# Kernel optimization log

Measured on AMD Instinct MI355X. Metric: run time of the kernel, lower is better.

## Reference

```python
import jax, jax.numpy as jnp
import numpy as np

B, S, H = 2, 2048, 2048
NQ, NKV = 32, 8          # query heads, kv heads
G = NQ // NKV            # query groups per kv head
D = H // NQ              # head dim = 64
MAX_POS = 4096
THETA = 10000.0


def _rope_tables(position_ids):
    # freqs per the original apply_rotary_emb (interleaved pair convention)
    freqs = 1.0 / THETA ** (jnp.arange(0, D, 2)[: D // 2].astype(jnp.float32) / D)
    t = jnp.arange(MAX_POS, dtype=jnp.float32)
    ang = jnp.outer(t, freqs)                     # [MAX_POS, D/2]
    cos = jnp.take(jnp.cos(ang), position_ids, axis=0)[:, :, None, :]  # [B,S,1,D/2]
    sin = jnp.take(jnp.sin(ang), position_ids, axis=0)[:, :, None, :]
    return cos, sin


def _apply_rope(x, cos, sin):
    # x: [B,S,h,D]; pairs are interleaved (x0,x1),(x2,x3),...
    x2 = x.astype(jnp.float32).reshape(*x.shape[:-1], D // 2, 2)
    xr, xi = x2[..., 0], x2[..., 1]
    out_r = xr * cos - xi * sin
    out_i = xr * sin + xi * cos
    return jnp.stack((out_r, out_i), axis=-1).reshape(x.shape).astype(x.dtype)


def setup_inputs() -> dict:
    key = jax.random.key(0)
    ks = jax.random.split(key, 5)
    init_scale = 0.02 / np.sqrt(H)
    hidden_states = jax.random.normal(ks[0], (B, S, H), dtype=jnp.float32)
    wq = jax.random.normal(ks[1], (H, H), dtype=jnp.float32) * init_scale
    wk = jax.random.normal(ks[2], (H, H // G), dtype=jnp.float32) * init_scale
    wv = jax.random.normal(ks[3], (H, H // G), dtype=jnp.float32) * init_scale
    wo = jax.random.normal(ks[4], (H, H), dtype=jnp.float32) * init_scale
    attention_mask = jnp.ones((B, S), dtype=jnp.int32)
    position_ids = jnp.broadcast_to(jnp.arange(S, dtype=jnp.int32), (B, S))
    return dict(hidden_states=hidden_states, attention_mask=attention_mask,
                position_ids=position_ids, wq=wq, wk=wk, wv=wv, wo=wo)


def reference(hidden_states, attention_mask, position_ids, wq, wk, wv, wo):
    # projections (no bias)
    xq = (hidden_states @ wq).reshape(B, S, NQ, D)
    xk = (hidden_states @ wk).reshape(B, S, NKV, D)
    xv = (hidden_states @ wv).reshape(B, S, NKV, D)
    # GQA repeat: kv head h -> query heads h*G .. h*G+G-1 (consecutive)
    xk = jnp.repeat(xk, G, axis=2)  # [B,S,NQ,D]
    xv = jnp.repeat(xv, G, axis=2)

    cos, sin = _rope_tables(position_ids)
    xq = _apply_rope(xq, cos, sin)
    xk = _apply_rope(xk, cos, sin)

    # causal + padding mask -> additive bias
    causal = jnp.tril(jnp.ones((S, S), dtype=bool))[None, None]          # [1,1,S,S]
    pad = (attention_mask > 0)[:, None, None, :]                          # [B,1,1,S]
    combined = jnp.logical_and(causal, pad)                               # [B,1,S,S]
    neg = jnp.finfo(jnp.float32).min
    bias = jnp.where(combined, 0.0, neg).astype(jnp.float32)

    scale = 1.0 / np.sqrt(D)
    scores = jnp.einsum('bqhd,bkhd->bhqk', xq, xk).astype(jnp.float32) * scale
    scores = scores + bias
    attn = jax.nn.softmax(scores, axis=-1)                                # [B,NQ,S,S] fp32
    out = jnp.einsum('bhqk,bkhd->bqhd', attn, xv)                         # [B,S,NQ,D]
    out = out.reshape(B, S, H)
    return out @ wo
```

## Files before the change

kernel.cpp:

```cpp
#include <hip/hip_runtime.h>
#include <cstdint>

typedef __attribute__((ext_vector_type(8))) __bf16  bf8v;
typedef __attribute__((ext_vector_type(4))) float   f4v;
typedef __attribute__((ext_vector_type(8))) unsigned short ush8;

__device__ __forceinline__ float bf2f(unsigned short u) {
    union { unsigned u; float f; } v; v.u = ((unsigned)u) << 16; return v.f;
}
__device__ __forceinline__ unsigned short f2bf(float f) {
    union { float f; unsigned u; } v; v.f = f;
    unsigned u = v.u;
    return (unsigned short)((u + 0x7fffu + ((u >> 16) & 1u)) >> 16);
}
__device__ __forceinline__ unsigned short f2bf_n(float f) {
    union { __bf16 h; unsigned short s; } v; v.h = (__bf16)f; return v.s;
}
__device__ __forceinline__ unsigned pack2bf(float a, float b) {
    union { __bf16 h[2]; unsigned u; } v;
    v.h[0] = (__bf16)a; v.h[1] = (__bf16)b; return v.u;
}

#define GLDS16(gp, lp)                                                          \
    __builtin_amdgcn_global_load_lds(                                           \
        (const __attribute__((address_space(1))) void*)(uintptr_t)(gp),         \
        (__attribute__((address_space(3))) void*)(uintptr_t)(lp), 16, 0, 0)

__global__ void cast_f32_to_bf16(const float* __restrict__ in,
                                 unsigned short* __restrict__ out, int n8) {
    int i = blockIdx.x * 256 + threadIdx.x;
    if (i >= n8) return;
    float4 a = ((const float4*)in)[2 * i];
    float4 b = ((const float4*)in)[2 * i + 1];
    ush8 o;
    o[0] = f2bf(a.x); o[1] = f2bf(a.y); o[2] = f2bf(a.z); o[3] = f2bf(a.w);
    o[4] = f2bf(b.x); o[5] = f2bf(b.y); o[6] = f2bf(b.z); o[7] = f2bf(b.w);
    ((ush8*)out)[i] = o;
}

__global__ void transpose_cast(const float* __restrict__ in,
                               unsigned short* __restrict__ out, int R, int C) {
    __shared__ float t[32][33];
    int c0 = blockIdx.x * 32, r0 = blockIdx.y * 32;
    int x = threadIdx.x, y = threadIdx.y;
    #pragma unroll
    for (int i = 0; i < 32; i += 8) t[y + i][x] = in[(size_t)(r0 + y + i) * C + c0 + x];
    __syncthreads();
    #pragma unroll
    for (int i = 0; i < 32; i += 8)
        out[(size_t)(c0 + y + i) * R + r0 + x] = f2bf(t[x][y + i]);
}

__global__ void transpose_v_bf16(const unsigned short* __restrict__ in,
                                 unsigned short* __restrict__ out) {
    __shared__ unsigned short t[32][33];
    int c0 = blockIdx.x * 32;
    int r0 = blockIdx.y * 32;
    int x = threadIdx.x, y = threadIdx.y;
    #pragma unroll
    for (int i = 0; i < 32; i += 8)
        t[y + i][x] = in[(size_t)(r0 + y + i) * 3072 + 2560 + c0 + x];
    __syncthreads();
    #pragma unroll
    for (int i = 0; i < 32; i += 8)
        out[(size_t)(c0 + y + i) * 4096 + r0 + x] = t[x][y + i];
}

__global__ void rope_strided(unsigned short* __restrict__ X,
                             const int* __restrict__ pos_ids,
                             int coloff, int stride, int nh_log2) {
    int idx = blockIdx.x * 256 + threadIdx.x;
    int i   = idx & 31;
    int hh  = (idx >> 5) & ((1 << nh_log2) - 1);
    int tok = idx >> (5 + nh_log2);
    int pos = pos_ids[tok];
    float ang = (float)pos * exp2f(-0.41524101186092f * (float)i);
    float s = sinf(ang), c = cosf(ang);
    unsigned short* p = X + (size_t)tok * stride + coloff + hh * 64 + 2 * i;
    unsigned pr = *(const unsigned*)p;
    float xr = bf2f((unsigned short)(pr & 0xffff));
    float xi = bf2f((unsigned short)(pr >> 16));
    float orr = xr * c - xi * s;
    float oi  = xr * s + xi * c;
    *(unsigned*)p = (unsigned)f2bf(orr) | ((unsigned)f2bf(oi) << 16);
}

template <int OUT_BF16>
__global__ __launch_bounds__(256) void gemm_bt(const unsigned short* __restrict__ A,
                                               const unsigned short* __restrict__ Bt,
                                               void* __restrict__ Cv, int N, int K) {
    __shared__ __align__(16) unsigned short As[128 * 64];
    __shared__ __align__(16) unsigned short Bs[128 * 64];
    const int t = threadIdx.x;
    const int lane = t & 63, w = t >> 6;
    const int wr = w >> 1, wc = w & 1;
    const int lr = lane & 15, lh = lane >> 4;
    const int m0 = blockIdx.y * 128, n0 = blockIdx.x * 128;

    f4v acc[4][4];
    #pragma unroll
    for (int i = 0; i < 4; ++i)
        #pragma unroll
        for (int j = 0; j < 4; ++j) acc[i][j] = f4v{0.f, 0.f, 0.f, 0.f};

    const int o_t = t * 16;
    for (int k0 = 0; k0 < K; k0 += 64) {
        __syncthreads();
        #pragma unroll
        for (int s = 0; s < 4; ++s) {
            int o = s * 4096 + o_t;
            int row = o >> 7;
            int src = (o & 127) ^ ((row & 7) << 4);
            const unsigned short* gA = A + (size_t)(m0 + row) * K + k0 + (src >> 1);
            GLDS16(gA, As + (o >> 1));
            const unsigned short* gB = Bt + (size_t)(n0 + row) * K + k0 + (src >> 1);
            GLDS16(gB, Bs + (o >> 1));
        }
        __syncthreads();
        #pragma unroll
        for (int kk = 0; kk < 2; ++kk) {
            bf8v af[4], bfr[4];
            #pragma unroll
            for (int mi = 0; mi < 4; ++mi) {
                int row = wr * 64 + mi * 16 + lr;
                int col = (kk * 32 + lh * 8) ^ ((row & 7) << 3);
                af[mi] = *(const bf8v*)(As + row * 64 + col);
            }
            #pragma unroll
            for (int ni = 0; ni < 4; ++ni) {
                int row = wc * 64 + ni * 16 + lr;
                int col = (kk * 32 + lh * 8) ^ ((row & 7) << 3);
                bfr[ni] = *(const bf8v*)(Bs + row * 64 + col);
            }
            #pragma unroll
            for (int mi = 0; mi < 4; ++mi)
                #pragma unroll
                for (int ni = 0; ni < 4; ++ni)
                    acc[mi][ni] = __builtin_amdgcn_mfma_f32_16x16x32_bf16(
                        af[mi], bfr[ni], acc[mi][ni], 0, 0, 0);
        }
    }
    #pragma unroll
    for (int mi = 0; mi < 4; ++mi)
        #pragma unroll
        for (int ni = 0; ni < 4; ++ni)
            #pragma unroll
            for (int r = 0; r < 4; ++r) {
                int row = m0 + wr * 64 + mi * 16 + lh * 4 + r;
                int col = n0 + wc * 64 + ni * 16 + lr;
                float v = acc[mi][ni][r];
                if (OUT_BF16) ((unsigned short*)Cv)[(size_t)row * N + col] = f2bf(v);
                else          ((float*)Cv)[(size_t)row * N + col] = v;
            }
}

__global__ __launch_bounds__(256, 4) void flash_attn(
        const unsigned short* __restrict__ QKV,
        const unsigned short* __restrict__ VtG,
        const int* __restrict__ amask,
        const int* __restrict__ pos_ids,
        unsigned short* __restrict__ O) {
    __shared__ __align__(16) unsigned short Ks[2][64 * 64];
    __shared__ __align__(16) unsigned short Vs[2][64 * 64];
    __shared__ __align__(16) unsigned short Ps[4][16 * 64];
    __shared__ int aliveT[32];

    const int t = threadIdx.x, lane = t & 63, w = t >> 6;
    const int lr = lane & 15, lh = lane >> 4;
    const int pair = blockIdx.x, h = blockIdx.y, b = blockIdx.z;
    const size_t tok0 = (size_t)b * 2048;

    const unsigned short* Kb = QKV + tok0 * 3072 + 2048 + (h >> 2) * 64;
    const unsigned short* Vb = VtG + (size_t)((h >> 2) * 64) * 4096 + tok0;
    const int* amrow = amask + b * 2048;

#define STAGE(buf, kt)                                                              \
    {   _Pragma("unroll")                                                           \
        for (int s_ = 0; s_ < 2; ++s_) {                                            \
            int c_ = s_ * 256 + t;                                                  \
            int row_ = c_ >> 3;                                                     \
            int sc_ = (((c_ & 7) * 16) ^ ((row_ & 7) << 4)) >> 1;                   \
            GLDS16(Kb + (size_t)((kt) * 64 + row_) * 3072 + sc_, Ks[buf] + c_ * 8); \
            GLDS16(Vb + (size_t)row_ * 4096 + (kt) * 64 + sc_, Vs[buf] + c_ * 8);   \
        }                                                                           \
    }

    const float SCL = 0.18033688011112042f;
    int cur = 0;

    if (t < 32) aliveT[t] = -1;
    __syncthreads();
    {
        const int4* am4 = (const int4*)amrow;
        int4 a0 = am4[2 * t], a1 = am4[2 * t + 1];
        int f = (a0.x && a0.y && a0.z && a0.w && a1.x && a1.y && a1.z && a1.w) ? -1 : 0;
        atomicAnd(&aliveT[t >> 3], f);
    }

    #pragma unroll 1
    for (int half = 0; half < 2; ++half) {
        const int qt = half ? (31 - pair) : pair;
        const int q0 = qt * 64;
        const int nkv = qt + 1;
        const int qloc = w * 16 + lr;

        const unsigned short* Qp = QKV + (tok0 + q0 + qloc) * 3072 + h * 64;
        union Q8 { bf8v v; unsigned short s[8]; } qa0u, qa1u;
        qa0u.v = *(const bf8v*)(Qp + lh * 8);
        qa1u.v = *(const bf8v*)(Qp + 32 + lh * 8);
        {
            int pos = pos_ids[tok0 + q0 + qloc];
            #pragma unroll
            for (int r = 0; r < 4; ++r) {
                float i0 = (float)(lh * 4 + r);
                float ang0 = (float)pos * exp2f(-0.41524101186092f * i0);
                float sn = sinf(ang0), cs = cosf(ang0);
                float xr = bf2f(qa0u.s[2 * r]), xi = bf2f(qa0u.s[2 * r + 1]);
                qa0u.s[2 * r]     = f2bf_n((xr * cs - xi * sn) * SCL);
                qa0u.s[2 * r + 1] = f2bf_n((xr * sn + xi * cs) * SCL);
                float i1 = (float)(16 + lh * 4 + r);
                float ang1 = (float)pos * exp2f(-0.41524101186092f * i1);
                float sn1 = sinf(ang1), cs1 = cosf(ang1);
                float yr = bf2f(qa1u.s[2 * r]), yi = bf2f(qa1u.s[2 * r + 1]);
                qa1u.s[2 * r]     = f2bf_n((yr * cs1 - yi * sn1) * SCL);
                qa1u.s[2 * r + 1] = f2bf_n((yr * sn1 + yi * cs1) * SCL);
            }
        }
        const bf8v qa0 = qa0u.v, qa1 = qa1u.v;

        f4v oacc[4];
        #pragma unroll
        for (int i = 0; i < 4; ++i) oacc[i] = f4v{0.f, 0.f, 0.f, 0.f};
        float m_ = -1e30f, l_ = 0.f;

        STAGE(cur, 0);
        __syncthreads();

        #pragma unroll 1
        for (int kt = 0; kt < nkv; ++kt) {
            if (kt + 1 < nkv) STAGE(cur ^ 1, kt + 1);

            f4v sa[4];
            #pragma unroll
            for (int kf = 0; kf < 4; ++kf) sa[kf] = f4v{0.f, 0.f, 0.f, 0.f};
            __builtin_amdgcn_s_setprio(1);
            #pragma unroll
            for (int kk = 0; kk < 2; ++kk) {
                bf8v qa = kk ? qa1 : qa0;
                int col = kk * 32 + lh * 8;
                #pragma unroll
                for (int kf = 0; kf < 4; ++kf) {
                    bf8v kb = *(const bf8v*)(Ks[cur] + (kf * 16 + lr) * 64 + (col ^ ((lr & 7) << 3)));
                    sa[kf] = __builtin_amdgcn_mfma_f32_16x16x32_bf16(kb, qa, sa[kf], 0, 0, 0);
                }
            }
            __builtin_amdgcn_s_setprio(0);

            const bool diag = (kt == qt);
            const bool tileAlive = (aliveT[kt] != 0);

            float pvv[4][4];
            if (tileAlive && !diag) {
                #pragma unroll
                for (int kf = 0; kf < 4; ++kf)
                    #pragma unroll
                    for (int r = 0; r < 4; ++r) pvv[kf][r] = sa[kf][r];
            } else if (tileAlive) {
                #pragma unroll
                for (int kf = 0; kf < 4; ++kf)
                    #pragma unroll
                    for (int r = 0; r < 4; ++r) {
                        int keyl = kf * 16 + lh * 4 + r;
                        pvv[kf][r] = (keyl > qloc) ? -1e30f : sa[kf][r];
                    }
            } else {
                int amv[4][4];
                #pragma unroll
                for (int kf = 0; kf < 4; ++kf) {
                    int4 aq = *(const int4*)(amrow + kt * 64 + kf * 16 + lh * 4);
                    amv[kf][0] = aq.x; amv[kf][1] = aq.y; amv[kf][2] = aq.z; amv[kf][3] = aq.w;
                }
                #pragma unroll
                for (int kf = 0; kf < 4; ++kf)
                    #pragma unroll
                    for (int r = 0; r < 4; ++r) {
                        int keyl = kf * 16 + lh * 4 + r;
                        bool dead = (amv[kf][r] == 0) || (diag && keyl > qloc);
                        pvv[kf][r] = dead ? -1e30f : sa[kf][r];
                    }
            }

            float t0 = fmaxf(fmaxf(pvv[0][0], pvv[0][1]), fmaxf(pvv[0][2], pvv[0][3]));
            float t1 = fmaxf(fmaxf(pvv[1][0], pvv[1][1]), fmaxf(pvv[1][2], pvv[1][3]));
            float t2 = fmaxf(fmaxf(pvv[2][0], pvv[2][1]), fmaxf(pvv[2][2], pvv[2][3]));
            float t3 = fmaxf(fmaxf(pvv[3][0], pvv[3][1]), fmaxf(pvv[3][2], pvv[3][3]));
            float mx = fmaxf(fmaxf(t0, t1), fmaxf(t2, t3));
            mx = fmaxf(mx, __shfl_xor(mx, 16));
            mx = fmaxf(mx, __shfl_xor(mx, 32));

            if (!__all(mx <= m_ + 8.0f)) {
                float mn = fmaxf(m_, mx);
                float fac = exp2f(m_ - mn);
                m_ = mn;
                l_ *= fac;
                float facr[4];
                #pragma unroll
                for (int r = 0; r < 4; ++r) facr[r] = __shfl(fac, lh * 4 + r);
                #pragma unroll
                for (int df = 0; df < 4; ++df) {
                    f4v o = oacc[df];
                    o[0] *= facr[0]; o[1] *= facr[1]; o[2] *= facr[2]; o[3] *= facr[3];
                    oacc[df] = o;
                }
            }

            float pe[4][4];
            #pragma unroll
            for (int kf = 0; kf < 4; ++kf)
                #pragma unroll
                for (int r = 0; r < 4; ++r)
                    pe[kf][r] = exp2f(pvv[kf][r] - m_);
            float s0 = (pe[0][0] + pe[0][1]) + (pe[0][2] + pe[0][3]);
            float s1 = (pe[1][0] + pe[1][1]) + (pe[1][2] + pe[1][3]);
            float s2 = (pe[2][0] + pe[2][1]) + (pe[2][2] + pe[2][3]);
            float s3 = (pe[3][0] + pe[3][1]) + (pe[3][2] + pe[3][3]);
            float rs = (s0 + s1) + (s2 + s3);
            rs += __shfl_xor(rs, 16);
            rs += __shfl_xor(rs, 32);
            l_ += rs;

            unsigned short* Pw = Ps[w];
            #pragma unroll
            for (int kf = 0; kf < 4; ++kf) {
                uint2 pk;
                pk.x = pack2bf(pe[kf][0], pe[kf][1]);
                pk.y = pack2bf(pe[kf][2], pe[kf][3]);
                int idx = lr * 64 + ((kf * 16 + lh * 4) ^ ((lr & 7) << 3));
                *(uint2*)(Pw + idx) = pk;
            }

            __builtin_amdgcn_s_setprio(1);
            #pragma unroll
            for (int kk = 0; kk < 2; ++kk) {
                int k0c = kk * 32 + lh * 8;
                bf8v pa = *(const bf8v*)(Pw + lr * 64 + (k0c ^ ((lr & 7) << 3)));
                #pragma unroll
                for (int df = 0; df < 4; ++df) {
                    int d = df * 16 + lr;
                    bf8v vb = *(const bf8v*)(Vs[cur] + d * 64 + (k0c ^ ((d & 7) << 3)));
                    oacc[df] = __builtin_amdgcn_mfma_f32_16x16x32_bf16(pa, vb, oacc[df], 0, 0, 0);
                }
            }
            __builtin_amdgcn_s_setprio(0);

            __syncthreads();
            cur ^= 1;
        }

        float invl = 1.0f / l_;
        float invr[4];
        #pragma unroll
        for (int r = 0; r < 4; ++r) invr[r] = __shfl(invl, lh * 4 + r);
        #pragma unroll
        for (int df = 0; df < 4; ++df)
            #pragma unroll
            for (int r = 0; r < 4; ++r) {
                int qg = q0 + w * 16 + lh * 4 + r;
                float v = oacc[df][r] * invr[r];
                O[(tok0 + qg) * 2048 + h * 64 + df * 16 + lr] = f2bf_n(v);
            }
    }
#undef STAGE
}

extern "C" void kernel_launch(void* const* d_in, const int* in_sizes, int n_in,
                              void* d_out, int out_size, void* d_ws, size_t ws_size,
                              hipStream_t stream) {
    const float* hs   = (const float*)d_in[0];
    const int* amask  = (const int*)d_in[1];
    const int* pos    = (const int*)d_in[2];
    const float* wq   = (const float*)d_in[3];
    const float* wk   = (const float*)d_in[4];
    const float* wv   = (const float*)d_in[5];
    const float* wo   = (const float*)d_in[6];

    char* ws = (char*)d_ws;
    unsigned short* Xb   = (unsigned short*)(ws);
    unsigned short* Wqkv = (unsigned short*)(ws + 16777216);
    unsigned short* Wot  = (unsigned short*)(ws + 29360128);
    unsigned short* AOb  = (unsigned short*)(ws + 37748736);

    char* ob = (char*)d_out;
    unsigned short* QKV = (unsigned short*)ob;
    unsigned short* VtG = (unsigned short*)(ob + 25165824);

    cast_f32_to_bf16<<<4096, 256, 0, stream>>>(hs, Xb, 1048576);
    transpose_cast<<<dim3(64, 64), dim3(32, 8), 0, stream>>>(wq, Wqkv, 2048, 2048);
    transpose_cast<<<dim3(16, 64), dim3(32, 8), 0, stream>>>(wk, Wqkv + 4194304, 2048, 512);
    transpose_cast<<<dim3(16, 64), dim3(32, 8), 0, stream>>>(wv, Wqkv + 5242880, 2048, 512);
    transpose_cast<<<dim3(64, 64), dim3(32, 8), 0, stream>>>(wo, Wot, 2048, 2048);

    gemm_bt<1><<<dim3(24, 32), 256, 0, stream>>>(Xb, Wqkv, (void*)QKV, 3072, 2048);

    rope_strided<<<4096, 256, 0, stream>>>(QKV, pos, 2048, 3072, 3);

    transpose_v_bf16<<<dim3(16, 128), dim3(32, 8), 0, stream>>>(QKV, VtG);

    flash_attn<<<dim3(16, 32, 2), 256, 0, stream>>>(QKV, VtG, amask, pos, AOb);

    gemm_bt<0><<<dim3(16, 32), 256, 0, stream>>>(AOb, Wot, d_out, 2048, 2048);
}
```

Measured before the change: 241.6 us.

## Feed P directly from registers via 16x16x16 MFMA, drop P LDS staging

```diff
diff --git a/kernel.cpp b/kernel.cpp
--- a/kernel.cpp
+++ b/kernel.cpp
@@ -3,6 +3,7 @@
 
 typedef __attribute__((ext_vector_type(8))) __bf16  bf8v;
 typedef __attribute__((ext_vector_type(4))) float   f4v;
+typedef __attribute__((ext_vector_type(4))) short   s4v;
 typedef __attribute__((ext_vector_type(8))) unsigned short ush8;
 
 __device__ __forceinline__ float bf2f(unsigned short u) {
@@ -154,7 +155,7 @@
             }
 }
 
-__global__ __launch_bounds__(256, 4) void flash_attn(
+__global__ __launch_bounds__(256, 5) void flash_attn(
         const unsigned short* __restrict__ QKV,
         const unsigned short* __restrict__ VtG,
         const int* __restrict__ amask,
@@ -162,8 +163,6 @@
         unsigned short* __restrict__ O) {
     __shared__ __align__(16) unsigned short Ks[2][64 * 64];
     __shared__ __align__(16) unsigned short Vs[2][64 * 64];
-    __shared__ __align__(16) unsigned short Ps[4][16 * 64];
-    __shared__ int aliveT[32];
 
     const int t = threadIdx.x, lane = t & 63, w = t >> 6;
     const int lr = lane & 15, lh = lane >> 4;
@@ -186,16 +185,27 @@
     }
 
     const float SCL = 0.18033688011112042f;
-    int cur = 0;
-
-    if (t < 32) aliveT[t] = -1;
-    __syncthreads();
+
+    unsigned aliveMaskV = 0;
     {
         const int4* am4 = (const int4*)amrow;
-        int4 a0 = am4[2 * t], a1 = am4[2 * t + 1];
-        int f = (a0.x && a0.y && a0.z && a0.w && a1.x && a1.y && a1.z && a1.w) ? -1 : 0;
-        atomicAnd(&aliveT[t >> 3], f);
+        #pragma unroll
+        for (int s = 0; s < 8; ++s) {
+            int4 a = am4[s * 64 + lane];
+            unsigned long long bal = __ballot(a.x && a.y && a.z && a.w);
+            #pragma unroll
+            for (int g = 0; g < 4; ++g)
+                aliveMaskV |= (((bal >> (16 * g)) & 0xFFFFull) == 0xFFFFull)
+                                  ? (1u << (4 * s + g)) : 0u;
+        }
     }
+    const int aliveMask = __builtin_amdgcn_readfirstlane((int)aliveMaskV);
+
+    int vcol[4];
+    #pragma unroll
+    for (int kf = 0; kf < 4; ++kf) vcol[kf] = (kf * 16 + lh * 4) ^ ((lr & 7) << 3);
+
+    int cur = 0;
 
     #pragma unroll 1
     for (int half = 0; half < 2; ++half) {
@@ -257,7 +267,7 @@
             __builtin_amdgcn_s_setprio(0);
 
             const bool diag = (kt == qt);
-            const bool tileAlive = (aliveT[kt] != 0);
+            const bool tileAlive = ((aliveMask >> kt) & 1) != 0;
 
             float pvv[4][4];
             if (tileAlive && !diag) {
@@ -329,26 +339,17 @@
             rs += __shfl_xor(rs, 32);
             l_ += rs;
 
-            unsigned short* Pw = Ps[w];
+            __builtin_amdgcn_s_setprio(1);
             #pragma unroll
             for (int kf = 0; kf < 4; ++kf) {
-                uint2 pk;
-                pk.x = pack2bf(pe[kf][0], pe[kf][1]);
-                pk.y = pack2bf(pe[kf][2], pe[kf][3]);
-                int idx = lr * 64 + ((kf * 16 + lh * 4) ^ ((lr & 7) << 3));
-                *(uint2*)(Pw + idx) = pk;
-            }
-
-            __builtin_amdgcn_s_setprio(1);
-            #pragma unroll
-            for (int kk = 0; kk < 2; ++kk) {
-                int k0c = kk * 32 + lh * 8;
-                bf8v pa = *(const bf8v*)(Pw + lr * 64 + (k0c ^ ((lr & 7) << 3)));
+                union { uint2 u; s4v s; } pa;
+                pa.u.x = pack2bf(pe[kf][0], pe[kf][1]);
+                pa.u.y = pack2bf(pe[kf][2], pe[kf][3]);
                 #pragma unroll
                 for (int df = 0; df < 4; ++df) {
-                    int d = df * 16 + lr;
-                    bf8v vb = *(const bf8v*)(Vs[cur] + d * 64 + (k0c ^ ((d & 7) << 3)));
-                    oacc[df] = __builtin_amdgcn_mfma_f32_16x16x32_bf16(pa, vb, oacc[df], 0, 0, 0);
+                    const s4v vb = *(const s4v*)(Vs[cur] + (df * 16 + lr) * 64 + vcol[kf]);
+                    oacc[df] = __builtin_amdgcn_mfma_f32_16x16x16bf16_1k(
+                        pa.s, vb, oacc[df], 0, 0, 0);
                 }
             }
             __builtin_amdgcn_s_setprio(0);
```

Result: no change. 237.4 us (-1.7%).
